# Kernel optimization log

Measured on AMD Instinct MI355X. Metric: run time of the kernel, lower is better.

The kernel has to match this reference:

```python
import jax, jax.numpy as jnp
import numpy as np

NHEADS = 16
LORA_SCALE = 16.0 / 16.0  # alpha / r


def lora_linear(x, W, b, A, B):
    # base projection + low-rank LoRA path: x@W^T + b + s*(x@A^T)@B^T
    base = jnp.einsum('bse,oe->bso', x, W) + b
    low = jnp.einsum('bse,re->bsr', x, A)  # [B,S,r]
    return base + LORA_SCALE * jnp.einsum('bsr,or->bso', low, B)


def setup_inputs() -> dict:
    key = jax.random.key(0)
    E, R = 1024, 16
    ks = jax.random.split(key, 20)
    d = {'x': jax.random.normal(ks[0], (4, 1024, E), jnp.float32)}
    i = 1
    for p in ('q', 'k', 'v', 'o'):
        d[f'{p}_w'] = jax.random.normal(ks[i], (E, E), jnp.float32) * 0.02; i += 1
        d[f'{p}_b'] = jax.random.normal(ks[i], (E,), jnp.float32) * 0.02; i += 1
        d[f'{p}_la'] = jax.random.normal(ks[i], (R, E), jnp.float32) * 0.02; i += 1
        d[f'{p}_lb'] = jax.random.normal(ks[i], (E, R), jnp.float32) * 0.02; i += 1
    return d


def reference(x, q_w, q_b, q_la, q_lb, k_w, k_b, k_la, k_lb,
              v_w, v_b, v_la, v_lb, o_w, o_b, o_la, o_lb):
    B, S, E = x.shape
    H = NHEADS
    D = E // H
    q = lora_linear(x, q_w, q_b, q_la, q_lb).reshape(B, S, H, D)
    k = lora_linear(x, k_w, k_b, k_la, k_lb).reshape(B, S, H, D)
    v = lora_linear(x, v_w, v_b, v_la, v_lb).reshape(B, S, H, D)
    scores = jnp.einsum('bshd,bthd->bhst', q, k) / jnp.sqrt(jnp.asarray(D, x.dtype))
    attn = jax.nn.softmax(scores, axis=-1)
    ctx = jnp.einsum('bhst,bthd->bshd', attn, v).reshape(B, S, E)
    return lora_linear(ctx, o_w, o_b, o_la, o_lb)
```

## Files before the change

### kernel.cpp

```cpp
#include <hip/hip_runtime.h>
#include <cstdint>


typedef __attribute__((ext_vector_type(8))) short bf16x8;
typedef __attribute__((ext_vector_type(4))) float f32x4;
typedef __attribute__((ext_vector_type(16))) float f32x16;
typedef __attribute__((ext_vector_type(4))) unsigned short u16x4;
typedef __attribute__((ext_vector_type(4))) unsigned int u32x4;

__device__ __forceinline__ short f2bf(float f) {
  unsigned u = __builtin_bit_cast(unsigned, f);
  u += 0x7FFFu + ((u >> 16) & 1u);
  return (short)(u >> 16);
}

typedef __attribute__((address_space(1))) const unsigned int as1_uint;
typedef __attribute__((address_space(3))) unsigned int as3_uint;

__device__ __forceinline__ void gload_lds16(const short* g, const short* l) {
  __builtin_amdgcn_global_load_lds((as1_uint*)g,
      (as3_uint*)(unsigned int)(uintptr_t)l, 16, 0, 0);
}

__device__ __forceinline__ unsigned cvtpk(float lo, float hi) {
  unsigned r;
  asm("v_cvt_pk_bf16_f32 %0, %1, %2" : "=v"(r) : "v"(lo), "v"(hi));
  return r;
}
__device__ __forceinline__ void plswap(unsigned &a, unsigned &b) {
  asm("v_permlane32_swap_b32 %0, %1" : "+v"(a), "+v"(b));
}

__device__ __forceinline__ void build_pfrag(const f32x16 &s, bf16x8 &f0, bf16x8 &f1) {
  unsigned x0 = cvtpk(s[0], s[1]),  x1 = cvtpk(s[2], s[3]);
  unsigned x2 = cvtpk(s[4], s[5]),  x3 = cvtpk(s[6], s[7]);
  plswap(x0, x2); plswap(x1, x3);
  unsigned y0 = cvtpk(s[8], s[9]),  y1 = cvtpk(s[10], s[11]);
  unsigned y2 = cvtpk(s[12], s[13]), y3 = cvtpk(s[14], s[15]);
  plswap(y0, y2); plswap(y1, y3);
  u32x4 a = {x0, x1, x2, x3}, b = {y0, y1, y2, y3};
  f0 = __builtin_bit_cast(bf16x8, a);
  f1 = __builtin_bit_cast(bf16x8, b);
}

__global__ void prep_kernel(const float* __restrict__ x, short* __restrict__ xb,
                            const float* __restrict__ wq, const float* __restrict__ wk,
                            const float* __restrict__ wv, const float* __restrict__ wo,
                            const float* __restrict__ bq, const float* __restrict__ bk,
                            const float* __restrict__ bv, const float* __restrict__ bo,
                            const float* __restrict__ aq, const float* __restrict__ ak,
                            const float* __restrict__ av, const float* __restrict__ ao,
                            short* __restrict__ wbo) {
  const int b = blockIdx.x;
  if (b < 4096) {
    const int idx = b * 256 + threadIdx.x;
    f32x4 v = ((const f32x4*)x)[idx];
    u16x4 o;
    o[0] = (unsigned short)f2bf(v[0]);
    o[1] = (unsigned short)f2bf(v[1]);
    o[2] = (unsigned short)f2bf(v[2]);
    o[3] = (unsigned short)f2bf(v[3]);
    ((u16x4*)xb)[idx] = o;
  } else {
    const int bb = b - 4096;
    const int p = bb >> 10;
    const float* W  = (p == 0) ? wq : (p == 1) ? wk : (p == 2) ? wv : wo;
    const float* Bm = (p == 0) ? bq : (p == 1) ? bk : (p == 2) ? bv : bo;
    const float* A  = (p == 0) ? aq : (p == 1) ? ak : (p == 2) ? av : ao;
    const int idx = (bb & 1023) * 256 + threadIdx.x;
    const int n = idx >> 8;
    const int e4 = idx & 255;
    f32x4 acc = ((const f32x4*)(W + (size_t)n * 1024))[e4];
    const float* br = Bm + n * 16;
    #pragma unroll
    for (int r = 0; r < 16; ++r) {
      const f32x4 a4 = ((const f32x4*)(A + (size_t)r * 1024))[e4];
      const float bl = br[r];
      acc[0] += bl * a4[0];
      acc[1] += bl * a4[1];
      acc[2] += bl * a4[2];
      acc[3] += bl * a4[3];
    }
    u16x4 o;
    o[0] = (unsigned short)f2bf(acc[0]);
    o[1] = (unsigned short)f2bf(acc[1]);
    o[2] = (unsigned short)f2bf(acc[2]);
    o[3] = (unsigned short)f2bf(acc[3]);
    *(u16x4*)(wbo + (size_t)p * 1048576 + (size_t)idx * 4) = o;
  }
}

__global__ __launch_bounds__(512, 2)
void gemm_qkv(const short* __restrict__ xb, const short* __restrict__ wb,
              const float* __restrict__ biasq, const float* __restrict__ biask,
              const float* __restrict__ biasv,
              short* __restrict__ qbuf, short* __restrict__ kbuf, short* __restrict__ vtb) {
  __shared__ short Ah[2][2][8192];
  __shared__ short Bh[2][2][8192];
  const int wg = blockIdx.x;
  const int swz = (wg & 7) * 24 + (wg >> 3);
  const int brow = swz / 12, bcol = swz % 12;
  const int tid = threadIdx.x;
  const int wid = tid >> 6, lane = tid & 63;
  const int wr = wid >> 2, wc = wid & 3;
  const int lrow = lane & 15, lk = lane >> 4;
  const int sl8 = (tid & 7) ^ ((tid >> 3) & 7);

  const short* Asrc = xb + (size_t)brow * 256 * 1024;
  const short* Bsrc = wb + (size_t)bcol * 256 * 1024;

#define STAGE_H(SRC, LDS, hf, kt, buf)                                         \
  { _Pragma("unroll")                                                          \
    for (int i = 0; i < 2; ++i) {                                              \
      const int row = (hf) * 128 + i * 64 + (tid >> 3);                        \
      gload_lds16(SRC + (size_t)row * 1024 + (kt) * 64 + sl8 * 8,              \
                  LDS[buf][hf] + (i * 64 + wid * 8) * 64);                     \
    } }

  const f32x4 fz = {0.f, 0.f, 0.f, 0.f};
  f32x4 acc[8][4];
  #pragma unroll
  for (int a = 0; a < 8; ++a)
    #pragma unroll
    for (int b = 0; b < 4; ++b) acc[a][b] = fz;

  STAGE_H(Asrc, Ah, 0, 0, 0)
  STAGE_H(Asrc, Ah, 1, 0, 0)
  STAGE_H(Bsrc, Bh, 0, 0, 0)
  STAGE_H(Bsrc, Bh, 1, 0, 0)
  STAGE_H(Bsrc, Bh, 0, 1, 1)
  STAGE_H(Bsrc, Bh, 1, 1, 1)
  asm volatile("s_waitcnt vmcnt(4)" ::: "memory");
  __builtin_amdgcn_s_barrier();

  const int bhalf = wc >> 1;
  for (int t = 0; t < 16; ++t) {
    const int cur = t & 1;
    bf16x8 bfr[4][2];
    #pragma unroll
    for (int q = 0; q < 4; ++q) {
      if (q == 0) {
        #pragma unroll
        for (int nj = 0; nj < 4; ++nj) {
          const int rr = (wc & 1) * 64 + nj * 16 + lrow;
          #pragma unroll
          for (int kc = 0; kc < 2; ++kc)
            bfr[nj][kc] = *(const bf16x8*)(&Bh[cur][bhalf][rr * 64 + (((kc * 4 + lk) ^ (rr & 7)) * 8)]);
        }
      }
      bf16x8 afr[2][2];
      #pragma unroll
      for (int m2 = 0; m2 < 2; ++m2) {
        const int rr = q * 32 + m2 * 16 + lrow;
        #pragma unroll
        for (int kc = 0; kc < 2; ++kc)
          afr[m2][kc] = *(const bf16x8*)(&Ah[cur][wr][rr * 64 + (((kc * 4 + lk) ^ (rr & 7)) * 8)]);
      }
      if (q == 0) { if (t + 1 < 16) STAGE_H(Asrc, Ah, 0, t + 1, cur ^ 1) }
      else if (q == 1) { if (t + 1 < 16) STAGE_H(Asrc, Ah, 1, t + 1, cur ^ 1) }
      else if (q == 2) { if (t + 2 < 16) STAGE_H(Bsrc, Bh, 0, t + 2, cur) }
      else             { if (t + 2 < 16) STAGE_H(Bsrc, Bh, 1, t + 2, cur) }

      if (q == 0) asm volatile("s_waitcnt lgkmcnt(8)" ::: "memory");
      __builtin_amdgcn_s_barrier();
      asm volatile("s_waitcnt lgkmcnt(0)" ::: "memory");
      __builtin_amdgcn_s_setprio(1);
      #pragma unroll
      for (int kc = 0; kc < 2; ++kc)
        #pragma unroll
        for (int m2 = 0; m2 < 2; ++m2)
          #pragma unroll
          for (int nj = 0; nj < 4; ++nj)
            acc[q * 2 + m2][nj] = __builtin_amdgcn_mfma_f32_16x16x32_bf16(
                afr[m2][kc], bfr[nj][kc], acc[q * 2 + m2][nj], 0, 0, 0);
      __builtin_amdgcn_s_setprio(0);
      if (q == 3) {
        if (t < 14) asm volatile("s_waitcnt vmcnt(4)" ::: "memory");
        else        asm volatile("s_waitcnt vmcnt(0)" ::: "memory");
      }
      __builtin_amdgcn_s_barrier();
    }
  }
#undef STAGE_H

  const int p = bcol >> 2;
  const float* bias = (p == 0) ? biasq : (p == 1) ? biask : biasv;
  const float oscale = (p == 0) ? 0.18033688f : 1.0f;
  const int c0 = (bcol & 3) * 256 + wc * 64;
  float bcv[4];
  #pragma unroll
  for (int nj = 0; nj < 4; ++nj)
    bcv[nj] = bias[c0 + nj * 16 + lrow];

  #pragma unroll
  for (int mi = 0; mi < 8; ++mi) {
    #pragma unroll
    for (int r = 0; r < 4; ++r) {
      const int gr = brow * 256 + wr * 128 + mi * 16 + lk * 4 + r;
      const int bb = gr >> 10, s = gr & 1023;
      #pragma unroll
      for (int nj = 0; nj < 4; ++nj) {
        const int gc = c0 + nj * 16 + lrow;
        const float v = (acc[mi][nj][r] + bcv[nj]) * oscale;
        const int h = gc >> 6, d = gc & 63;
        const int bh = bb * 16 + h;
        if (p == 2)
          vtb[((size_t)bh * 64 + d) * 1024 + s] = f2bf(v);
        else
          ((p == 0) ? qbuf : kbuf)[((size_t)bh * 1024 + s) * 64 + d] = f2bf(v);
      }
    }
  }
}

__global__ __launch_bounds__(512)
void attn_kernel(const short* __restrict__ qbuf, const short* __restrict__ kbuf,
                 const short* __restrict__ vtb, short* __restrict__ cb) {
  __shared__ short Ks[3][64 * 64];
  __shared__ short Vs[3][64 * 64];
  const int bh = blockIdx.x, qt = blockIdx.y;
  const int tid = threadIdx.x, w = tid >> 6, lane = tid & 63;
  const int l31 = lane & 31, hi = lane >> 5;
  const int srow = lane >> 3, sphys = lane & 7;
  const short* Qp = qbuf + (size_t)bh * 65536;
  const short* Kp = kbuf + (size_t)bh * 65536;
  const short* Vp = vtb + (size_t)bh * 65536;
  const int q0 = qt * 256 + w * 32;

  bf16x8 bq[4];
  #pragma unroll
  for (int kc = 0; kc < 4; ++kc)
    bq[kc] = *(const bf16x8*)(Qp + (size_t)(q0 + l31) * 64 + kc * 16 + hi * 8);

  const f32x16 fz16 = {0.f,0.f,0.f,0.f,0.f,0.f,0.f,0.f,0.f,0.f,0.f,0.f,0.f,0.f,0.f,0.f};
  float m_run = -1e30f, l_run = 0.f;
  f32x16 acc0 = fz16, acc1 = fz16;

  #define STAGE_KV(buf, tt)                                                  \
    {                                                                        \
      const int t0s = (tt) * 64;                                             \
      const int row = w * 8 + srow;                                          \
      const int sl = sphys ^ (row & 7);                                      \
      gload_lds16(Kp + (size_t)(t0s + row) * 64 + sl * 8, Ks[buf] + w * 512); \
      gload_lds16(Vp + (size_t)row * 1024 + t0s + sl * 8, Vs[buf] + w * 512); \
    }

  STAGE_KV(0, 0);

  int cur = 0, nxt = 1;
  for (int tt = 0; tt < 16; ++tt) {
    if (tt < 15) {
      STAGE_KV(nxt, tt + 1);
      asm volatile("s_waitcnt vmcnt(2)" ::: "memory");
    } else {
      asm volatile("s_waitcnt vmcnt(0)" ::: "memory");
    }
    asm volatile("s_waitcnt lgkmcnt(0)" ::: "memory");
    __builtin_amdgcn_s_barrier();

    f32x16 s0 = fz16, s1 = fz16;
    __builtin_amdgcn_s_setprio(1);
    #pragma unroll
    for (int kc = 0; kc < 4; ++kc) {
      const int slot = (kc * 2 + hi) ^ (l31 & 7);
      const bf16x8 ak0 = *(const bf16x8*)(Ks[cur] + l31 * 64 + slot * 8);
      const bf16x8 ak1 = *(const bf16x8*)(Ks[cur] + (32 + l31) * 64 + slot * 8);
      s0 = __builtin_amdgcn_mfma_f32_32x32x16_bf16(ak0, bq[kc], s0, 0, 0, 0);
      s1 = __builtin_amdgcn_mfma_f32_32x32x16_bf16(ak1, bq[kc], s1, 0, 0, 0);
    }
    __builtin_amdgcn_s_setprio(0);

    float t16[16];
    #pragma unroll
    for (int r = 0; r < 8; ++r) t16[r] = fmaxf(s0[2 * r], s0[2 * r + 1]);
    #pragma unroll
    for (int r = 0; r < 8; ++r) t16[8 + r] = fmaxf(s1[2 * r], s1[2 * r + 1]);
    #pragma unroll
    for (int r = 0; r < 8; ++r) t16[r] = fmaxf(t16[r], t16[r + 8]);
    #pragma unroll
    for (int r = 0; r < 4; ++r) t16[r] = fmaxf(t16[r], t16[r + 4]);
    float tm = fmaxf(fmaxf(t16[0], t16[1]), fmaxf(t16[2], t16[3]));
    tm = fmaxf(tm, __shfl_xor(tm, 32, 64));

    if (__any(tm - m_run > 8.0f)) {
      const float mn = fmaxf(m_run, tm);
      const float alpha = exp2f(m_run - mn);
      m_run = mn;
      l_run *= alpha;
      #pragma unroll
      for (int r = 0; r < 16; ++r) { acc0[r] *= alpha; acc1[r] *= alpha; }
    }

    float a16[16];
    #pragma unroll
    for (int r = 0; r < 16; ++r) { s0[r] = exp2f(s0[r] - m_run); }
    #pragma unroll
    for (int r = 0; r < 16; ++r) { s1[r] = exp2f(s1[r] - m_run); }
    #pragma unroll
    for (int r = 0; r < 8; ++r) a16[r] = s0[2 * r] + s0[2 * r + 1];
    #pragma unroll
    for (int r = 0; r < 8; ++r) a16[8 + r] = s1[2 * r] + s1[2 * r + 1];
    #pragma unroll
    for (int r = 0; r < 8; ++r) a16[r] += a16[r + 8];
    #pragma unroll
    for (int r = 0; r < 4; ++r) a16[r] += a16[r + 4];
    float rs = (a16[0] + a16[1]) + (a16[2] + a16[3]);
    rs += __shfl_xor(rs, 32, 64);
    l_run += rs;

    bf16x8 pf[4];
    build_pfrag(s0, pf[0], pf[1]);
    build_pfrag(s1, pf[2], pf[3]);

    __builtin_amdgcn_s_setprio(1);
    #pragma unroll
    for (int kc4 = 0; kc4 < 4; ++kc4) {
      const int slot = (kc4 * 2 + hi) ^ (l31 & 7);
      const bf16x8 av0 = *(const bf16x8*)(Vs[cur] + l31 * 64 + slot * 8);
      const bf16x8 av1 = *(const bf16x8*)(Vs[cur] + (32 + l31) * 64 + slot * 8);
      acc0 = __builtin_amdgcn_mfma_f32_32x32x16_bf16(av0, pf[kc4], acc0, 0, 0, 0);
      acc1 = __builtin_amdgcn_mfma_f32_32x32x16_bf16(av1, pf[kc4], acc1, 0, 0, 0);
    }
    __builtin_amdgcn_s_setprio(0);

    cur = (cur == 2) ? 0 : (cur + 1);
    nxt = (nxt == 2) ? 0 : (nxt + 1);
  }

  const int bb = bh >> 4, h = bh & 15;
  const int s = q0 + l31;
  short* crow = cb + (size_t)(bb * 1024 + s) * 1024 + h * 64;
  const float inv = 1.f / l_run;
  #pragma unroll
  for (int rp = 0; rp < 8; ++rp) {
    const int r = rp * 2;
    const int d = (r & 3) + 8 * (r >> 2) + 4 * hi;
    const unsigned p0 = (unsigned)(unsigned short)f2bf(acc0[r] * inv)
                      | ((unsigned)(unsigned short)f2bf(acc0[r + 1] * inv) << 16);
    const unsigned p1 = (unsigned)(unsigned short)f2bf(acc1[r] * inv)
                      | ((unsigned)(unsigned short)f2bf(acc1[r + 1] * inv) << 16);
    *(unsigned*)(crow + d) = p0;
    *(unsigned*)(crow + 32 + d) = p1;
  }
  #undef STAGE_KV
}

__device__ __forceinline__ void gemm_core_p3(const short* __restrict__ xrow,
                                             const short* __restrict__ wrow,
                                             short (&As)[3][8192], short (&Bs)[3][8192],
                                             f32x4 (&acc)[4][4]) {
  const int tid = threadIdx.x;
  const int wv = tid >> 6, lane = tid & 63;
  const int wr = wv >> 1, wc = wv & 1;
  const int lrow = lane & 15, lk = lane >> 4;
  const int srow = lane >> 3, sphys = lane & 7;

#define STAGE_G(buf, kt)                                                       \
  {                                                                            \
    _Pragma("unroll")                                                          \
    for (int i = 0; i < 4; ++i) {                                              \
      const int ch = i * 4 + wv;                                               \
      const int row = ch * 8 + srow;                                           \
      const int sl = sphys ^ (row & 7);                                        \
      gload_lds16(xrow + (size_t)row * 1024 + (kt) * 64 + sl * 8, As[buf] + ch * 512); \
      gload_lds16(wrow + (size_t)row * 1024 + (kt) * 64 + sl * 8, Bs[buf] + ch * 512); \
    }                                                                          \
  }

  STAGE_G(0, 0);
  STAGE_G(1, 1);
  int cur = 0;
  for (int kt = 0; kt < 16; ++kt) {
    if (kt < 14) {
      const int nb = (cur == 0) ? 2 : (cur - 1);
      STAGE_G(nb, kt + 2);
      asm volatile("s_waitcnt vmcnt(16)" ::: "memory");
    } else if (kt == 14) {
      asm volatile("s_waitcnt vmcnt(8)" ::: "memory");
    } else {
      asm volatile("s_waitcnt vmcnt(0)" ::: "memory");
    }
    __builtin_amdgcn_s_barrier();

    #pragma unroll
    for (int kc = 0; kc < 2; ++kc) {
      bf16x8 af[4], bw[4];
      #pragma unroll
      for (int mi = 0; mi < 4; ++mi) {
        const int row = wr * 64 + mi * 16 + lrow;
        const int slot = (kc * 4 + lk) ^ (row & 7);
        af[mi] = *(const bf16x8*)(As[cur] + row * 64 + slot * 8);
      }
      #pragma unroll
      for (int nj = 0; nj < 4; ++nj) {
        const int row = wc * 64 + nj * 16 + lrow;
        const int slot = (kc * 4 + lk) ^ (row & 7);
        bw[nj] = *(const bf16x8*)(Bs[cur] + row * 64 + slot * 8);
      }
      __builtin_amdgcn_s_setprio(1);
      #pragma unroll
      for (int mi = 0; mi < 4; ++mi)
        #pragma unroll
        for (int nj = 0; nj < 4; ++nj)
          acc[mi][nj] = __builtin_amdgcn_mfma_f32_16x16x32_bf16(af[mi], bw[nj], acc[mi][nj], 0, 0, 0);
      __builtin_amdgcn_s_setprio(0);
    }

    asm volatile("s_waitcnt lgkmcnt(0)" ::: "memory");
    __builtin_amdgcn_s_barrier();
    cur = (cur == 2) ? 0 : (cur + 1);
  }
#undef STAGE_G
}

__global__ __launch_bounds__(256)
void gemm_o(const short* __restrict__ cb, const short* __restrict__ wo,
            const float* __restrict__ biaso, float* __restrict__ out) {
  __shared__ short As[3][8192];
  __shared__ short Bs[3][8192];
  const int brow = blockIdx.y, bcol = blockIdx.x;
  const f32x4 fz = {0.f, 0.f, 0.f, 0.f};
  f32x4 acc[4][4];
  #pragma unroll
  for (int a = 0; a < 4; ++a)
    #pragma unroll
    for (int b = 0; b < 4; ++b) acc[a][b] = fz;

  gemm_core_p3(cb + (size_t)brow * 128 * 1024, wo + (size_t)bcol * 128 * 1024,
               As, Bs, acc);

  const int tid = threadIdx.x;
  const int wv = tid >> 6, lane = tid & 63;
  const int wr = wv >> 1, wc = wv & 1;
  const int lrow = lane & 15, lk = lane >> 4;
  float bcv[4];
  #pragma unroll
  for (int nj = 0; nj < 4; ++nj)
    bcv[nj] = biaso[bcol * 128 + wc * 64 + nj * 16 + lrow];

  #pragma unroll
  for (int mi = 0; mi < 4; ++mi) {
    #pragma unroll
    for (int r = 0; r < 4; ++r) {
      const int gr = brow * 128 + wr * 64 + mi * 16 + lk * 4 + r;
      #pragma unroll
      for (int nj = 0; nj < 4; ++nj) {
        const int gc = bcol * 128 + wc * 64 + nj * 16 + lrow;
        out[(size_t)gr * 1024 + gc] = acc[mi][nj][r] + bcv[nj];
      }
    }
  }
}

extern "C" void kernel_launch(void* const* d_in, const int* in_sizes, int n_in,
                              void* d_out, int out_size, void* d_ws, size_t ws_size,
                              hipStream_t stream) {
  (void)in_sizes; (void)n_in; (void)out_size; (void)ws_size;
  const float* x   = (const float*)d_in[0];
  const float* qw  = (const float*)d_in[1];
  const float* qb  = (const float*)d_in[2];
  const float* qla = (const float*)d_in[3];
  const float* qlb = (const float*)d_in[4];
  const float* kw  = (const float*)d_in[5];
  const float* kb  = (const float*)d_in[6];
  const float* kla = (const float*)d_in[7];
  const float* klb = (const float*)d_in[8];
  const float* vw  = (const float*)d_in[9];
  const float* vb  = (const float*)d_in[10];
  const float* vla = (const float*)d_in[11];
  const float* vlb = (const float*)d_in[12];
  const float* ow  = (const float*)d_in[13];
  const float* ob  = (const float*)d_in[14];
  const float* ola = (const float*)d_in[15];
  const float* olb = (const float*)d_in[16];

  short* xb   = (short*)d_ws;
  short* wb   = xb + (size_t)4096 * 1024;
  short* qbuf = wb + (size_t)4 * 1024 * 1024;
  short* kbuf = qbuf + (size_t)4194304;
  short* vtb  = kbuf + (size_t)4194304;

  prep_kernel<<<8192, 256, 0, stream>>>(x, xb, qw, kw, vw, ow,
                                        qlb, klb, vlb, olb,
                                        qla, kla, vla, ola, wb);
  gemm_qkv<<<192, 512, 0, stream>>>(xb, wb, qb, kb, vb, qbuf, kbuf, vtb);
  attn_kernel<<<dim3(64, 4), 512, 0, stream>>>(qbuf, kbuf, vtb, xb);
  gemm_o<<<dim3(8, 32), 256, 0, stream>>>(xb, wb + (size_t)3 * 1024 * 1024, ob, (float*)d_out);
}
```

Before: 128.6 us.

## Retile QKV GEMM to 256x192 tiles so 256 workgroups fill all CUs

The fused QKV GEMM changes its output tile from 256x256 to 256x192, which raises the grid from 192 to 256 workgroups and matches the 256 CUs. The B-operand staging, LDS layout, wait counts and epilogue are reworked for the 192-wide tile. Since a tile can now cross the q/k/v boundary, bias and scale are picked per column. Each workgroup does less reuse per loaded A tile, and launch bounds drop to one block per CU.

```diff
diff --git a/kernel.cpp b/kernel.cpp
--- a/kernel.cpp
+++ b/kernel.cpp
@@ -90,16 +90,16 @@
   }
 }
 
-__global__ __launch_bounds__(512, 2)
+__global__ __launch_bounds__(512, 1)
 void gemm_qkv(const short* __restrict__ xb, const short* __restrict__ wb,
               const float* __restrict__ biasq, const float* __restrict__ biask,
               const float* __restrict__ biasv,
               short* __restrict__ qbuf, short* __restrict__ kbuf, short* __restrict__ vtb) {
   __shared__ short Ah[2][2][8192];
-  __shared__ short Bh[2][2][8192];
+  __shared__ short Bf[2][12288];
   const int wg = blockIdx.x;
-  const int swz = (wg & 7) * 24 + (wg >> 3);
-  const int brow = swz / 12, bcol = swz % 12;
+  const int swz = (wg & 7) * 32 + (wg >> 3);
+  const int brow = swz >> 4, bcol = swz & 15;
   const int tid = threadIdx.x;
   const int wid = tid >> 6, lane = tid & 63;
   const int wr = wid >> 2, wc = wid & 3;
@@ -107,45 +107,48 @@
   const int sl8 = (tid & 7) ^ ((tid >> 3) & 7);
 
   const short* Asrc = xb + (size_t)brow * 256 * 1024;
-  const short* Bsrc = wb + (size_t)bcol * 256 * 1024;
-
-#define STAGE_H(SRC, LDS, hf, kt, buf)                                         \
+  const short* Bsrc = wb + (size_t)bcol * 192 * 1024;
+
+#define STAGE_A(hf, kt, buf)                                                   \
   { _Pragma("unroll")                                                          \
     for (int i = 0; i < 2; ++i) {                                              \
       const int row = (hf) * 128 + i * 64 + (tid >> 3);                        \
-      gload_lds16(SRC + (size_t)row * 1024 + (kt) * 64 + sl8 * 8,              \
-                  LDS[buf][hf] + (i * 64 + wid * 8) * 64);                     \
+      gload_lds16(Asrc + (size_t)row * 1024 + (kt) * 64 + sl8 * 8,             \
+                  Ah[buf][hf] + (i * 64 + wid * 8) * 64);                      \
     } }
+#define STAGE_B(ch, kt, buf)                                                   \
+  {                                                                            \
+    const int row = (ch) * 64 + (tid >> 3);                                    \
+    gload_lds16(Bsrc + (size_t)row * 1024 + (kt) * 64 + sl8 * 8,               \
+                Bf[buf] + (ch) * 4096 + tid * 8);                              \
+  }
 
   const f32x4 fz = {0.f, 0.f, 0.f, 0.f};
-  f32x4 acc[8][4];
+  f32x4 acc[8][3];
   #pragma unroll
   for (int a = 0; a < 8; ++a)
     #pragma unroll
-    for (int b = 0; b < 4; ++b) acc[a][b] = fz;
-
-  STAGE_H(Asrc, Ah, 0, 0, 0)
-  STAGE_H(Asrc, Ah, 1, 0, 0)
-  STAGE_H(Bsrc, Bh, 0, 0, 0)
-  STAGE_H(Bsrc, Bh, 1, 0, 0)
-  STAGE_H(Bsrc, Bh, 0, 1, 1)
-  STAGE_H(Bsrc, Bh, 1, 1, 1)
-  asm volatile("s_waitcnt vmcnt(4)" ::: "memory");
+    for (int b = 0; b < 3; ++b) acc[a][b] = fz;
+
+  STAGE_A(0, 0, 0)
+  STAGE_A(1, 0, 0)
+  STAGE_B(0, 0, 0) STAGE_B(1, 0, 0) STAGE_B(2, 0, 0)
+  STAGE_B(0, 1, 1) STAGE_B(1, 1, 1) STAGE_B(2, 1, 1)
+  asm volatile("s_waitcnt vmcnt(3)" ::: "memory");
   __builtin_amdgcn_s_barrier();
 
-  const int bhalf = wc >> 1;
   for (int t = 0; t < 16; ++t) {
     const int cur = t & 1;
-    bf16x8 bfr[4][2];
+    bf16x8 bfr[3][2];
     #pragma unroll
     for (int q = 0; q < 4; ++q) {
       if (q == 0) {
         #pragma unroll
-        for (int nj = 0; nj < 4; ++nj) {
-          const int rr = (wc & 1) * 64 + nj * 16 + lrow;
+        for (int nj = 0; nj < 3; ++nj) {
+          const int rr = wc * 48 + nj * 16 + lrow;
           #pragma unroll
           for (int kc = 0; kc < 2; ++kc)
-            bfr[nj][kc] = *(const bf16x8*)(&Bh[cur][bhalf][rr * 64 + (((kc * 4 + lk) ^ (rr & 7)) * 8)]);
+            bfr[nj][kc] = *(const bf16x8*)(&Bf[cur][rr * 64 + (((kc * 4 + lk) ^ (rr & 7)) * 8)]);
         }
       }
       bf16x8 afr[2][2];
@@ -156,12 +159,12 @@
         for (int kc = 0; kc < 2; ++kc)
           afr[m2][kc] = *(const bf16x8*)(&Ah[cur][wr][rr * 64 + (((kc * 4 + lk) ^ (rr & 7)) * 8)]);
       }
-      if (q == 0) { if (t + 1 < 16) STAGE_H(Asrc, Ah, 0, t + 1, cur ^ 1) }
-      else if (q == 1) { if (t + 1 < 16) STAGE_H(Asrc, Ah, 1, t + 1, cur ^ 1) }
-      else if (q == 2) { if (t + 2 < 16) STAGE_H(Bsrc, Bh, 0, t + 2, cur) }
-      else             { if (t + 2 < 16) STAGE_H(Bsrc, Bh, 1, t + 2, cur) }
-
-      if (q == 0) asm volatile("s_waitcnt lgkmcnt(8)" ::: "memory");
+      if (q == 0)      { if (t + 1 < 16) STAGE_A(0, t + 1, cur ^ 1) }
+      else if (q == 1) { if (t + 1 < 16) STAGE_A(1, t + 1, cur ^ 1) }
+      else if (q == 2) { if (t + 2 < 16) { STAGE_B(0, t + 2, cur) STAGE_B(1, t + 2, cur) } }
+      else             { if (t + 2 < 16) STAGE_B(2, t + 2, cur) }
+
+      if (q == 0) asm volatile("s_waitcnt lgkmcnt(6)" ::: "memory");
       __builtin_amdgcn_s_barrier();
       asm volatile("s_waitcnt lgkmcnt(0)" ::: "memory");
       __builtin_amdgcn_s_setprio(1);
@@ -170,28 +173,21 @@
         #pragma unroll
         for (int m2 = 0; m2 < 2; ++m2)
           #pragma unroll
-          for (int nj = 0; nj < 4; ++nj)
+          for (int nj = 0; nj < 3; ++nj)
             acc[q * 2 + m2][nj] = __builtin_amdgcn_mfma_f32_16x16x32_bf16(
                 afr[m2][kc], bfr[nj][kc], acc[q * 2 + m2][nj], 0, 0, 0);
       __builtin_amdgcn_s_setprio(0);
       if (q == 3) {
-        if (t < 14) asm volatile("s_waitcnt vmcnt(4)" ::: "memory");
+        if (t < 14) asm volatile("s_waitcnt vmcnt(3)" ::: "memory");
         else        asm volatile("s_waitcnt vmcnt(0)" ::: "memory");
       }
       __builtin_amdgcn_s_barrier();
     }
   }
-#undef STAGE_H
-
-  const int p = bcol >> 2;
-  const float* bias = (p == 0) ? biasq : (p == 1) ? biask : biasv;
-  const float oscale = (p == 0) ? 0.18033688f : 1.0f;
-  const int c0 = (bcol & 3) * 256 + wc * 64;
-  float bcv[4];
-  #pragma unroll
-  for (int nj = 0; nj < 4; ++nj)
-    bcv[nj] = bias[c0 + nj * 16 + lrow];
-
+#undef STAGE_A
+#undef STAGE_B
+
+  const float SCALE = 0.18033688f;
   #pragma unroll
   for (int mi = 0; mi < 8; ++mi) {
     #pragma unroll
@@ -199,10 +195,12 @@
       const int gr = brow * 256 + wr * 128 + mi * 16 + lk * 4 + r;
       const int bb = gr >> 10, s = gr & 1023;
       #pragma unroll
-      for (int nj = 0; nj < 4; ++nj) {
-        const int gc = c0 + nj * 16 + lrow;
-        const float v = (acc[mi][nj][r] + bcv[nj]) * oscale;
-        const int h = gc >> 6, d = gc & 63;
+      for (int nj = 0; nj < 3; ++nj) {
+        const int gc = bcol * 192 + wc * 48 + nj * 16 + lrow;
+        const int p = gc >> 10, pc = gc & 1023;
+        const float bv = ((p == 0) ? biasq : (p == 1) ? biask : biasv)[pc];
+        const float v = (acc[mi][nj][r] + bv) * ((p == 0) ? SCALE : 1.0f);
+        const int h = pc >> 6, d = pc & 63;
         const int bh = bb * 16 + h;
         if (p == 2)
           vtb[((size_t)bh * 64 + d) * 1024 + s] = f2bf(v);
@@ -483,7 +481,7 @@
   prep_kernel<<<8192, 256, 0, stream>>>(x, xb, qw, kw, vw, ow,
                                         qlb, klb, vlb, olb,
                                         qla, kla, vla, ola, wb);
-  gemm_qkv<<<192, 512, 0, stream>>>(xb, wb, qb, kb, vb, qbuf, kbuf, vtb);
+  gemm_qkv<<<256, 512, 0, stream>>>(xb, wb, qb, kb, vb, qbuf, kbuf, vtb);
   attn_kernel<<<dim3(64, 4), 512, 0, stream>>>(qbuf, kbuf, vtb, xb);
   gemm_o<<<dim3(8, 32), 256, 0, stream>>>(xb, wb + (size_t)3 * 1024 * 1024, ob, (float*)d_out);
 }
```

New measurement: 121.7 us. 5.3% less time.
